# Kernel tuning notes

Hardware: AMD Instinct MI355X
Metric: run time of the kernel (lower is better)

## Reference

```python
import jax, jax.numpy as jnp
import numpy as np
from jax import lax

B, C, T = 64, 122, 500
COUT, D, H, FF, L = 64, 128, 8, 256, 2
NSUB, NCLS = 13, 4
EPS = 1e-5


def _gelu(x):
    return jax.nn.gelu(x, approximate=False)  # torch nn.GELU default (erf)


def _bn(x, g, b, m, v):
    # eval-mode BatchNorm1d over channel dim of [N, C, T]
    scale = (g / jnp.sqrt(v + EPS))[None, :, None]
    return (x - m[None, :, None]) * scale + b[None, :, None]


def _ln(x, g, b):
    mu = x.mean(-1, keepdims=True)
    var = ((x - mu) ** 2).mean(-1, keepdims=True)
    return (x - mu) / jnp.sqrt(var + EPS) * g + b


def _conv1d(x, w, b, pad):
    y = lax.conv_general_dilated(x, w, (1,), [(pad, pad)], dimension_numbers=('NCH', 'OIH', 'NCH'))
    return y + b[None, :, None]


def forward(x, subject_ids, conv1_w, conv1_b, bn1_g, bn1_b, bn1_m, bn1_v,
            conv2_w, conv2_b, bn2_g, bn2_b, bn2_m, bn2_v,
            proj_w, proj_b, elec_emb,
            qkv_w, qkv_b, out_w, out_b, ln1_g, ln1_b,
            ff1_w, ff1_b, ff2_w, ff2_b, ln2_g, ln2_b,
            heads_w, heads_b):
    bsz = x.shape[0]
    h = x.reshape(bsz * C, 1, T)                               # [B*C, 1, T]
    h = _gelu(_bn(_conv1d(h, conv1_w, conv1_b, 4), bn1_g, bn1_b, bn1_m, bn1_v))
    h = h.reshape(bsz * C, COUT, T // 2, 2).max(-1)            # MaxPool1d(2)
    h = _gelu(_bn(_conv1d(h, conv2_w, conv2_b, 2), bn2_g, bn2_b, bn2_m, bn2_v))
    h = h.mean(-1)                                             # AdaptiveAvgPool1d(1)
    tok = h @ proj_w.T + proj_b                                # [B*C, D]
    tok = tok.reshape(bsz, C, D) + elec_emb[:, :C, :]
    dh = D // H
    inv_sqrt_dh = 1.0 / float(np.sqrt(dh))
    for l in range(L):  # post-norm TransformerEncoderLayer, gelu activation
        qkv = jnp.einsum('bsd,ed->bse', tok, qkv_w[l]) + qkv_b[l]
        q, k, v = jnp.split(qkv, 3, axis=-1)
        q = q.reshape(bsz, C, H, dh)
        k = k.reshape(bsz, C, H, dh)
        v = v.reshape(bsz, C, H, dh)
        att = jax.nn.softmax(jnp.einsum('bqhd,bkhd->bhqk', q, k) * inv_sqrt_dh, axis=-1)
        ctx = jnp.einsum('bhqk,bkhd->bqhd', att, v).reshape(bsz, C, D)
        tok = _ln(tok + ctx @ out_w[l].T + out_b[l], ln1_g[l], ln1_b[l])
        ff = _gelu(tok @ ff1_w[l].T + ff1_b[l]) @ ff2_w[l].T + ff2_b[l]
        tok = _ln(tok + ff, ln2_g[l], ln2_b[l])
    pooled = tok.mean(axis=1)                                  # [B, D]
    # per-subject head routing == gather subject's weight/bias, batched matvec
    hw = heads_w[subject_ids]                                  # [B, NCLS, D]
    hb = heads_b[subject_ids]                                  # [B, NCLS]
    return jnp.einsum('bd,bcd->bc', pooled, hw) + hb


def setup_inputs() -> dict:
    key = jax.random.key(0)
    ks = jax.random.split(key, 16)
    def n(i, shape, s=0.02):
        return jax.random.normal(ks[i], shape, jnp.float32) * s
    return {
        'x': jax.random.normal(ks[0], (B, C, T), jnp.float32),
        'subject_ids': jax.random.randint(ks[1], (B,), 0, NSUB),
        'conv1_w': n(2, (COUT, 1, 9), 0.3), 'conv1_b': jnp.zeros((COUT,), jnp.float32),
        'bn1_g': jnp.ones((COUT,), jnp.float32), 'bn1_b': jnp.zeros((COUT,), jnp.float32),
        'bn1_m': jnp.zeros((COUT,), jnp.float32), 'bn1_v': jnp.ones((COUT,), jnp.float32),
        'conv2_w': n(3, (COUT, COUT, 5), 0.05), 'conv2_b': jnp.zeros((COUT,), jnp.float32),
        'bn2_g': jnp.ones((COUT,), jnp.float32), 'bn2_b': jnp.zeros((COUT,), jnp.float32),
        'bn2_m': jnp.zeros((COUT,), jnp.float32), 'bn2_v': jnp.ones((COUT,), jnp.float32),
        'proj_w': n(4, (D, COUT), 0.05), 'proj_b': jnp.zeros((D,), jnp.float32),
        'elec_emb': n(5, (1, C, D), 0.02),
        'qkv_w': n(6, (L, 3 * D, D), 0.05), 'qkv_b': jnp.zeros((L, 3 * D), jnp.float32),
        'out_w': n(7, (L, D, D), 0.05), 'out_b': jnp.zeros((L, D), jnp.float32),
        'ln1_g': jnp.ones((L, D), jnp.float32), 'ln1_b': jnp.zeros((L, D), jnp.float32),
        'ff1_w': n(8, (L, FF, D), 0.05), 'ff1_b': jnp.zeros((L, FF), jnp.float32),
        'ff2_w': n(9, (L, D, FF), 0.05), 'ff2_b': jnp.zeros((L, D), jnp.float32),
        'ln2_g': jnp.ones((L, D), jnp.float32), 'ln2_b': jnp.zeros((L, D), jnp.float32),
        'heads_w': n(10, (NSUB, NCLS, D), 0.05), 'heads_b': jnp.zeros((NSUB, NCLS), jnp.float32),
    }


def reference(x, subject_ids, conv1_w, conv1_b, bn1_g, bn1_b, bn1_m, bn1_v,
              conv2_w, conv2_b, bn2_g, bn2_b, bn2_m, bn2_v,
              proj_w, proj_b, elec_emb,
              qkv_w, qkv_b, out_w, out_b, ln1_g, ln1_b,
              ff1_w, ff1_b, ff2_w, ff2_b, ln2_g, ln2_b,
              heads_w, heads_b):
    return forward(x, subject_ids, conv1_w, conv1_b, bn1_g, bn1_b, bn1_m, bn1_v,
                   conv2_w, conv2_b, bn2_g, bn2_b, bn2_m, bn2_v,
                   proj_w, proj_b, elec_emb,
                   qkv_w, qkv_b, out_w, out_b, ln1_g, ln1_b,
                   ff1_w, ff1_b, ff2_w, ff2_b, ln2_g, ln2_b,
                   heads_w, heads_b)
```

## Files before the change

### kernel.cpp

```cpp
#include <hip/hip_runtime.h>
#include <hip/hip_fp16.h>
#include <hip/hip_bf16.h>
#include <math.h>

#define BB 64
#define CC 122
#define TT 500
#define NCOUT 64
#define DD 128
#define HHEADS 8
#define FFDIM 256
#define NLAYER 2
#define EPS 1e-5f
#define SEQ (BB*CC)

#define WS_W2T     0u
#define WS_PWT     10240u
#define WS_S1      20480u
#define WS_SH1     20544u
#define WS_S2      20608u
#define WS_SH2     20672u
#define WS_WBF     20736u
#define WS_TOK     151808u
#define WS_QKVB    1151232u
#define WS_VTB     2150656u
#define WS_GTAB    2674944u
#define WS_W1S     2675968u
#define WS_QKVB2   2676992u
#define WS_VTB2    3676416u

#define WB_QKV  0u
#define WB_OUT  98304u
#define WB_FF1  131072u
#define WB_FF2  196608u

typedef __attribute__((ext_vector_type(8))) short bf16x8;
typedef __attribute__((ext_vector_type(4))) float f32x4;

__device__ __forceinline__ unsigned short f2bf(float f) {
    unsigned int u = __float_as_uint(f);
    unsigned int r = u + 0x7FFFu + ((u >> 16) & 1u);
    return (unsigned short)(r >> 16);
}

__device__ __forceinline__ unsigned pk_bf16(float a, float b) {
    float r;
    asm("v_cvt_pk_bf16_f32 %0, %1, %2" : "=v"(r) : "v"(a), "v"(b));
    return __float_as_uint(r);
}
__device__ __forceinline__ unsigned short f2bf_hw(float f) {
    return (unsigned short)pk_bf16(f, f);
}

__device__ __forceinline__ float gelu_fast(float x) {
    float z = fabsf(x) * 0.70710678118654752f;
    float t = __builtin_amdgcn_rcpf(fmaf(0.3275911f, z, 1.0f));
    float p = fmaf(fmaf(fmaf(fmaf(1.061405429f, t, -1.453152027f), t,
                             1.421413741f), t, -0.284496736f), t, 0.254829592f);
    float e = __expf(-z * z);
    float erf_abs = fmaf(-p * t, e, 1.0f);
    float erf_x = copysignf(erf_abs, x);
    return 0.5f * x * (1.0f + erf_x);
}

__device__ __forceinline__ float gelu_idx(float p, const unsigned* __restrict__ gt) {
    p = fminf(fmaxf(p, 0.0f), 511.999f);
    int i = (int)p;
    float fr = p - (float)i;
    unsigned u = gt[i];
    __half2 h2 = *(__half2*)&u;
    float v0 = __half2float(h2.x);
    float d  = __half2float(h2.y);
    return fmaf(fr, d, v0);
}

__device__ __forceinline__ int swz3(int r) {
    return (r & 7) ^ (((r >> 4) & 1) << 1) ^ (((r >> 5) & 1) << 2);
}

__global__ void prep_kernel(const float* __restrict__ conv1_w, const float* __restrict__ conv1_b,
                            const float* __restrict__ bn1_g, const float* __restrict__ bn1_b,
                            const float* __restrict__ bn1_m, const float* __restrict__ bn1_v,
                            const float* __restrict__ conv2_w, const float* __restrict__ conv2_b,
                            const float* __restrict__ bn2_g, const float* __restrict__ bn2_b,
                            const float* __restrict__ bn2_m, const float* __restrict__ bn2_v,
                            const float* __restrict__ qkv_w, const float* __restrict__ out_w,
                            const float* __restrict__ ff1_w, const float* __restrict__ ff2_w,
                            const float* __restrict__ proj_w,
                            float* __restrict__ ws) {
    int idx = blockIdx.x * blockDim.x + threadIdx.x;
    if (idx < 20480) {
        int ci = idx & 63; int co = (idx >> 6) & 63; int kk = idx >> 12;
        unsigned short* wt = (unsigned short*)(ws + WS_W2T);
        wt[idx] = f2bf(conv2_w[(co*64 + ci)*5 + kk]);
    } else if (idx < 20544) {
        int i = idx - 20480;
        float s = bn1_g[i] * rsqrtf(bn1_v[i] + EPS);
        ws[WS_S1 + i] = s;
        ws[WS_SH1 + i] = (conv1_b[i] - bn1_m[i]) * s + bn1_b[i];
    } else if (idx < 20608) {
        int i = idx - 20544;
        float s = bn2_g[i] * rsqrtf(bn2_v[i] + EPS);
        ws[WS_S2 + i] = s;
        ws[WS_SH2 + i] = (conv2_b[i] - bn2_m[i]) * s + bn2_b[i];
    } else if (idx < 282752) {
        int r = idx - 20608;
        unsigned short* wbf = (unsigned short*)(ws + WS_WBF);
        float v;
        if (r < 98304)       v = qkv_w[r];
        else if (r < 131072) v = out_w[r - 98304];
        else if (r < 196608) v = ff1_w[r - 131072];
        else                 v = ff2_w[r - 196608];
        wbf[r] = f2bf(v);
    } else if (idx < 283264) {
        int i = idx - 282752;
        float x0 = (i - 256) * 0.03125f;
        float x1 = x0 + 0.03125f;
        float g0 = 0.5f*x0*(1.0f + erff(x0*0.70710678118654752f));
        float g1 = 0.5f*x1*(1.0f + erff(x1*0.70710678118654752f));
        __half hv = __float2half_rn(g0);
        __half hd = __float2half_rn(g1 - g0);
        unsigned short uv = *(unsigned short*)&hv;
        unsigned short ud = *(unsigned short*)&hd;
        ((unsigned*)(ws + WS_GTAB))[i] = (unsigned)uv | ((unsigned)ud << 16);
    } else if (idx < 285312) {
        int i = idx - 283264;
        int co = i >> 5, k = i & 31;
        unsigned short* w1s = (unsigned short*)(ws + WS_W1S);
        float s = bn1_g[co] * rsqrtf(bn1_v[co] + EPS);
        w1s[i] = (k < 9) ? f2bf(conv1_w[co*9 + k] * s) : (unsigned short)0;
    } else if (idx < 293504) {
        int i = idx - 285312;
        int o = i >> 7, d = i & 127;
        ws[WS_PWT + i] = proj_w[d*64 + o];
    }
}

__global__ __launch_bounds__(256, 4) void conv_kernel(const float* __restrict__ x,
            const float* __restrict__ proj_b,
            const float* __restrict__ elec,
            const float* __restrict__ wsr, float* __restrict__ tok) {
    __shared__ __align__(16) unsigned short h1s[264*64];
    __shared__ __align__(16) unsigned short xbf[544];
    __shared__ __align__(16) unsigned gtab[512];
    __shared__ float part[256];
    __shared__ float mean_l[64];
    int n = blockIdx.x;
    int c = n % CC;
    int tid = threadIdx.x;
    const float* xg = x + (size_t)n * TT;

    for (int i = tid; i < 544; i += 256) {
        unsigned short v = 0;
        if (i >= 4 && i < 504) v = f2bf_hw(xg[i-4]);
        xbf[i] = v;
    }
    if (tid < 128) {
        ((uint4*)gtab)[tid] = ((const uint4*)(wsr + WS_GTAB))[tid];
    }
    for (int idx = tid; idx < 14*64; idx += 256) {
        int rr = idx >> 6;
        int r = (rr < 2) ? rr : (rr - 2 + 252);
        h1s[r*64 + (idx & 63)] = 0;
    }
    __syncthreads();

    int lane = tid & 63;
    int w = tid >> 6;
    int ln15 = lane & 15, lg = lane >> 4;

    {
        const unsigned short* w1s = (const unsigned short*)(wsr + WS_W1S);
        bf16x8 b1f[4];
        float shp[4];
#pragma unroll
        for (int nt = 0; nt < 4; nt++) {
            int co = nt*16 + ln15;
            b1f[nt] = *(const bf16x8*)&w1s[co*32 + lg*8];
            shp[nt] = fmaf(wsr[WS_SH1 + co], 32.0f, 256.0f);
        }
        int P = w*128 + ln15*8 + lg*8;
        uint4 Va = *(const uint4*)&xbf[P];
        uint4 Vb = *(const uint4*)&xbf[P + 8];
        unsigned vwin[8] = {Va.x, Va.y, Va.z, Va.w, Vb.x, Vb.y, Vb.z, Vb.w};
#pragma unroll
        for (int a = 0; a < 4; a++) {
            union { unsigned u[4]; bf16x8 b; } Ue, Uo;
#pragma unroll
            for (int d = 0; d < 4; d++) {
                Ue.u[d] = vwin[a + d];
                Uo.u[d] = (vwin[a + d] >> 16) | (vwin[a + d + 1] << 16);
            }
            f32x4 ce[4], cod[4];
#pragma unroll
            for (int nt = 0; nt < 4; nt++) {
                ce[nt]  = __builtin_amdgcn_mfma_f32_16x16x32_bf16(Ue.b, b1f[nt],
                              (f32x4){0.f,0.f,0.f,0.f}, 0, 0, 0);
                cod[nt] = __builtin_amdgcn_mfma_f32_16x16x32_bf16(Uo.b, b1f[nt],
                              (f32x4){0.f,0.f,0.f,0.f}, 0, 0, 0);
            }
#pragma unroll
            for (int nt = 0; nt < 4; nt++) {
                int co = nt*16 + ln15;
#pragma unroll
                for (int i = 0; i < 4; i++) {
                    int tp = w*64 + lg*16 + i*4 + a;
                    if (tp < 250) {
                        float ge = gelu_idx(fmaf(ce[nt][i],  32.0f, shp[nt]), gtab);
                        float go = gelu_idx(fmaf(cod[nt][i], 32.0f, shp[nt]), gtab);
                        int r = tp + 2;
                        int cp = (co >> 3) ^ swz3(r);
                        h1s[r*64 + cp*8 + (co & 7)] = f2bf_hw(fmaxf(ge, go));
                    }
                }
            }
        }
    }
    __syncthreads();

    const unsigned short* wt = (const unsigned short*)(wsr + WS_W2T);
    f32x4 acc[4][4];
#pragma unroll
    for (int mi = 0; mi < 4; mi++)
#pragma unroll
        for (int nt = 0; nt < 4; nt++) acc[mi][nt] = (f32x4){0.f, 0.f, 0.f, 0.f};

    const unsigned short* wbase = wt + ln15*64 + lg*8;
#pragma unroll
    for (int kk = 0; kk < 5; kk++) {
#pragma unroll
        for (int s = 0; s < 2; s++) {
            bf16x8 bfv[4];
#pragma unroll
            for (int nt = 0; nt < 4; nt++)
                bfv[nt] = *(const bf16x8*)(wbase + kk*4096 + nt*1024 + s*32);
#pragma unroll
            for (int mi = 0; mi < 4; mi++) {
                int r = (w*4 + mi)*16 + ln15 + kk;
                int cp = (s*4 + lg) ^ swz3(r);
                bf16x8 af = *(const bf16x8*)&h1s[r*64 + cp*8];
#pragma unroll
                for (int nt = 0; nt < 4; nt++)
                    acc[mi][nt] = __builtin_amdgcn_mfma_f32_16x16x32_bf16(af, bfv[nt], acc[mi][nt], 0, 0, 0);
            }
        }
    }

#pragma unroll
    for (int nt = 0; nt < 4; nt++) {
        int co2 = nt*16 + ln15;
        float sc = wsr[WS_S2 + co2] * 32.0f;
        float sh = fmaf(wsr[WS_SH2 + co2], 32.0f, 256.0f);
        float p = 0.f;
#pragma unroll
        for (int mi = 0; mi < 4; mi++) {
            int tbase = (w*4 + mi)*16 + lg*4;
#pragma unroll
            for (int i = 0; i < 4; i++) {
                if (tbase + i < 250)
                    p += gelu_idx(fmaf(acc[mi][nt][i], sc, sh), gtab);
            }
        }
        p += __shfl_down(p, 32, 64);
        p += __shfl_down(p, 16, 64);
        if (lane < 16) part[w*64 + co2] = p;
    }
    __syncthreads();
    if (tid < 64) {
        mean_l[tid] = (part[tid] + part[64+tid] + part[128+tid] + part[192+tid]) * (1.0f/250.0f);
    }
    __syncthreads();

    if (tid < DD) {
        int d = tid;
        const float* pwt = wsr + WS_PWT;
        float a = proj_b[d] + elec[c*DD + d];
#pragma unroll 8
        for (int o = 0; o < 64; o++) a = fmaf(mean_l[o], pwt[o*128 + d], a);
        tok[(size_t)n * DD + d] = a;
    }
}

__global__ __launch_bounds__(256) void qkv_gemm(const float* __restrict__ Aptr,
        const unsigned short* __restrict__ Bbf,
        const float* __restrict__ bias,
        unsigned short* __restrict__ qkvb,
        unsigned short* __restrict__ vtb) {
    const int tid = threadIdx.x;
    const int m0 = blockIdx.x * 32;
    const int y  = blockIdx.y;
    const int n0 = y * 128;
    __shared__ __align__(16) unsigned short As[32*128];

    const float* A = Aptr + (size_t)m0 * 128;
    for (int i = tid; i < 1024; i += 256) {
        int m = i >> 5; int kq = (i & 31)*4;
        float4 v = *(const float4*)(A + m*128 + kq);
        int cp = (kq >> 3) ^ (m & 15);
        unsigned p0 = pk_bf16(v.x, v.y);
        unsigned p1 = pk_bf16(v.z, v.w);
        *(uint2*)&As[m*128 + cp*8 + (kq & 7)] = make_uint2(p0, p1);
    }
    __syncthreads();

    const int lane = tid & 63, w = tid >> 6;
    const int ln15 = lane & 15, lg = lane >> 4;
    f32x4 acc[2][2];
#pragma unroll
    for (int mi = 0; mi < 2; mi++)
#pragma unroll
        for (int ni = 0; ni < 2; ni++) acc[mi][ni] = (f32x4){0.f, 0.f, 0.f, 0.f};

    const unsigned short* Bb = Bbf + (size_t)n0 * 128;
#pragma unroll
    for (int kt = 0; kt < 4; kt++) {
        bf16x8 af[2], bfv[2];
#pragma unroll
        for (int mi = 0; mi < 2; mi++) {
            int m = mi*16 + ln15;
            int cp = (kt*4 + lg) ^ (m & 15);
            af[mi] = *(const bf16x8*)&As[m*128 + cp*8];
        }
#pragma unroll
        for (int ni = 0; ni < 2; ni++) {
            int nn = (w*2 + ni)*16 + ln15;
            bfv[ni] = *(const bf16x8*)&Bb[(size_t)nn*128 + kt*32 + lg*8];
        }
#pragma unroll
        for (int mi = 0; mi < 2; mi++)
#pragma unroll
            for (int ni = 0; ni < 2; ni++)
                acc[mi][ni] = __builtin_amdgcn_mfma_f32_16x16x32_bf16(af[mi], bfv[ni], acc[mi][ni], 0, 0, 0);
    }

#pragma unroll
    for (int mi = 0; mi < 2; mi++)
#pragma unroll
        for (int ni = 0; ni < 2; ni++) {
            int nloc = (w*2 + ni)*16 + ln15;
            float bb = bias[n0 + nloc];
#pragma unroll
            for (int i = 0; i < 4; i++) {
                int ml = mi*16 + lg*4 + i;
                int nrow = m0 + ml;
                unsigned short us = f2bf_hw(acc[mi][ni][i] + bb);
                if (y < 2) {
                    qkvb[(size_t)nrow*256 + n0 + nloc] = us;
                } else {
                    int bq = nrow / 122;
                    int j  = nrow - bq*122;
                    vtb[((size_t)(bq*128 + nloc))*128 + j] = us;
                }
            }
        }
}

__global__ __launch_bounds__(512) void attn_tail(
        const unsigned short* __restrict__ qkvb,
        const unsigned short* __restrict__ vtb,
        const unsigned short* __restrict__ outW, const float* __restrict__ outb,
        float* __restrict__ tok,
        const float* __restrict__ ln1g, const float* __restrict__ ln1b,
        const unsigned short* __restrict__ B1, const float* __restrict__ b1,
        const unsigned short* __restrict__ B2, const float* __restrict__ b2,
        const float* __restrict__ ln2g, const float* __restrict__ ln2b,
        const unsigned short* __restrict__ Bq, const float* __restrict__ bq,
        unsigned short* __restrict__ qkvb_o, unsigned short* __restrict__ vtb_o,
        int do_qkv) {
    __shared__ float Cs[16*129];
    __shared__ __align__(16) unsigned short Pregion[8*16*128];
    __shared__ __align__(16) unsigned short ctxs[16*128];

    const int tid = threadIdx.x;
    const int blk = blockIdx.x;
    const int b = blk >> 3, mq = blk & 7;
    const int m0l = mq * 16;
    const int lane = tid & 63, w = tid >> 6;
    const int ln15 = lane & 15, lg = lane >> 4;

    const unsigned short* qb = qkvb + (size_t)b * 122 * 256;
    unsigned short* Pw = Pregion + w * 2048;

    {
        const int h = w;
        int mrow = m0l + ln15;
        int gr = (mrow < 122) ? mrow : 121;
        bf16x8 af = {0,0,0,0,0,0,0,0};
        if (lg < 2) af = *(const bf16x8*)(qb + gr*256 + h*16 + lg*8);
        f32x4 S[8];
#pragma unroll
        for (int nt = 0; nt < 8; nt++) {
            int j = nt*16 + ln15;
            int gj = (j < 122) ? j : 121;
            bf16x8 bv = {0,0,0,0,0,0,0,0};
            if (lg < 2) bv = *(const bf16x8*)(qb + gj*256 + 128 + h*16 + lg*8);
            S[nt] = __builtin_amdgcn_mfma_f32_16x16x32_bf16(af, bv,
                        (f32x4){0.f,0.f,0.f,0.f}, 0, 0, 0);
        }
        float sm[4];
#pragma unroll
        for (int i = 0; i < 4; i++) {
            float m_ = -1e30f;
#pragma unroll
            for (int nt = 0; nt < 8; nt++) {
                float v = S[nt][i] * 0.25f;
                if (nt == 7 && ln15 >= 10) v = -1e30f;
                S[nt][i] = v;
                m_ = fmaxf(m_, v);
            }
            m_ = fmaxf(m_, __shfl_xor(m_, 1, 64));
            m_ = fmaxf(m_, __shfl_xor(m_, 2, 64));
            m_ = fmaxf(m_, __shfl_xor(m_, 4, 64));
            m_ = fmaxf(m_, __shfl_xor(m_, 8, 64));
            float s_ = 0.f;
#pragma unroll
            for (int nt = 0; nt < 8; nt++) {
                float e = __expf(S[nt][i] - m_);
                S[nt][i] = e;
                s_ += e;
            }
            s_ += __shfl_xor(s_, 1, 64);
            s_ += __shfl_xor(s_, 2, 64);
            s_ += __shfl_xor(s_, 4, 64);
            s_ += __shfl_xor(s_, 8, 64);
            sm[i] = s_;
        }
#pragma unroll
        for (int nt = 0; nt < 8; nt++)
#pragma unroll
            for (int i = 0; i < 4; i++) {
                int rp = lg*4 + i;
                int j = nt*16 + ln15;
                int cp = (j >> 3) ^ rp;
                Pw[rp*128 + cp*8 + (j & 7)] = f2bf_hw(S[nt][i]);
            }
        f32x4 cacc = (f32x4){0.f,0.f,0.f,0.f};
#pragma unroll
        for (int kt = 0; kt < 4; kt++) {
            bf16x8 bv = *(const bf16x8*)(vtb + ((size_t)(b*128 + h*16 + ln15))*128 + kt*32 + lg*8);
            int m = ln15;
            int cp = (kt*4 + lg) ^ m;
            bf16x8 ap = *(const bf16x8*)&Pw[m*128 + cp*8];
            cacc = __builtin_amdgcn_mfma_f32_16x16x32_bf16(ap, bv, cacc, 0, 0, 0);
        }
#pragma unroll
        for (int i = 0; i < 4; i++) {
            float inv = __builtin_amdgcn_rcpf(sm[i]);
            int rp = lg*4 + i;
            int ccol = h*16 + ln15;
            int cp = (ccol >> 3) ^ (rp & 15);
            ctxs[rp*128 + cp*8 + (ccol & 7)] = f2bf_hw(cacc[i] * inv);
        }
    }
    __syncthreads();

    {
        f32x4 acc = (f32x4){0.f,0.f,0.f,0.f};
        int nn = w*16 + ln15;
#pragma unroll
        for (int kt = 0; kt < 4; kt++) {
            bf16x8 bv = *(const bf16x8*)&outW[(size_t)nn*128 + kt*32 + lg*8];
            int m = ln15;
            int cp = (kt*4 + lg) ^ (m & 15);
            bf16x8 afm = *(const bf16x8*)&ctxs[m*128 + cp*8];
            acc = __builtin_amdgcn_mfma_f32_16x16x32_bf16(afm, bv, acc, 0, 0, 0);
        }
        float bb = outb[nn];
#pragma unroll
        for (int i = 0; i < 4; i++) {
            int ml = lg*4 + i;
            int mrow = m0l + ml;
            int grow = b*122 + ((mrow < 122) ? mrow : 121);
            Cs[ml*129 + nn] = acc[i] + bb + tok[(size_t)grow*128 + nn];
        }
    }
    __syncthreads();

    unsigned short* ln1buf = Pregion;
    unsigned short* Hs = Pregion + 2048;
    {
        int r = tid >> 5, sub = tid & 31;
        float s1 = 0.f, s2 = 0.f;
#pragma unroll
        for (int j = 0; j < 4; j++) {
            float vv = Cs[r*129 + sub*4 + j];
            s1 += vv; s2 += vv*vv;
        }
        s1 += __shfl_xor(s1, 1, 64);  s2 += __shfl_xor(s2, 1, 64);
        s1 += __shfl_xor(s1, 2, 64);  s2 += __shfl_xor(s2, 2, 64);
        s1 += __shfl_xor(s1, 4, 64);  s2 += __shfl_xor(s2, 4, 64);
        s1 += __shfl_xor(s1, 8, 64);  s2 += __shfl_xor(s2, 8, 64);
        s1 += __shfl_xor(s1, 16, 64); s2 += __shfl_xor(s2, 16, 64);
        float mu = s1 * (1.0f/128.0f);
        float var = s2 * (1.0f/128.0f) - mu*mu;
        float rstd = rsqrtf(var + EPS);
#pragma unroll
        for (int j = 0; j < 4; j++) {
            int nloc = sub*4 + j;
            float vv = (Cs[r*129 + nloc] - mu) * rstd * ln1g[nloc] + ln1b[nloc];
            Cs[r*129 + nloc] = vv;
            int cp = (nloc >> 3) ^ (r & 15);
            ln1buf[r*128 + cp*8 + (nloc & 7)] = f2bf_hw(vv);
        }
    }
    __syncthreads();

    {
        f32x4 acc1[2];
#pragma unroll
        for (int ni = 0; ni < 2; ni++) acc1[ni] = (f32x4){0.f,0.f,0.f,0.f};
#pragma unroll
        for (int kt = 0; kt < 4; kt++) {
            int m = ln15;
            int cp = (kt*4 + lg) ^ (m & 15);
            bf16x8 afm = *(const bf16x8*)&ln1buf[m*128 + cp*8];
#pragma unroll
            for (int ni = 0; ni < 2; ni++) {
                int nn = (w*2 + ni)*16 + ln15;
                bf16x8 bv = *(const bf16x8*)&B1[(size_t)nn*128 + kt*32 + lg*8];
                acc1[ni] = __builtin_amdgcn_mfma_f32_16x16x32_bf16(afm, bv, acc1[ni], 0, 0, 0);
            }
        }
#pragma unroll
        for (int ni = 0; ni < 2; ni++) {
            int nn = (w*2 + ni)*16 + ln15;
            float bb = b1[nn];
#pragma unroll
            for (int i = 0; i < 4; i++) {
                int m = lg*4 + i;
                float v = gelu_fast(acc1[ni][i] + bb);
                int cp = (nn >> 3) ^ (m & 15);
                Hs[m*256 + cp*8 + (nn & 7)] = f2bf_hw(v);
            }
        }
    }
    __syncthreads();

    {
        f32x4 acc2 = (f32x4){0.f,0.f,0.f,0.f};
        int nn = w*16 + ln15;
#pragma unroll
        for (int kt = 0; kt < 8; kt++) {
            bf16x8 bv = *(const bf16x8*)&B2[(size_t)nn*256 + kt*32 + lg*8];
            int m = ln15;
            int cp = (kt*4 + lg) ^ (m & 15);
            bf16x8 afm = *(const bf16x8*)&Hs[m*256 + cp*8];
            acc2 = __builtin_amdgcn_mfma_f32_16x16x32_bf16(afm, bv, acc2, 0, 0, 0);
        }
        float bb = b2[nn];
#pragma unroll
        for (int i = 0; i < 4; i++) {
            int ml = lg*4 + i;
            Cs[ml*129 + nn] = acc2[i] + bb + Cs[ml*129 + nn];
        }
    }
    __syncthreads();

    {
        int r = tid >> 5, sub = tid & 31;
        float s1 = 0.f, s2 = 0.f;
#pragma unroll
        for (int j = 0; j < 4; j++) {
            float vv = Cs[r*129 + sub*4 + j];
            s1 += vv; s2 += vv*vv;
        }
        s1 += __shfl_xor(s1, 1, 64);  s2 += __shfl_xor(s2, 1, 64);
        s1 += __shfl_xor(s1, 2, 64);  s2 += __shfl_xor(s2, 2, 64);
        s1 += __shfl_xor(s1, 4, 64);  s2 += __shfl_xor(s2, 4, 64);
        s1 += __shfl_xor(s1, 8, 64);  s2 += __shfl_xor(s2, 8, 64);
        s1 += __shfl_xor(s1, 16, 64); s2 += __shfl_xor(s2, 16, 64);
        float mu = s1 * (1.0f/128.0f);
        float var = s2 * (1.0f/128.0f) - mu*mu;
        float rstd = rsqrtf(var + EPS);
        bool rowok = (m0l + r < 122);
#pragma unroll
        for (int j = 0; j < 4; j++) {
            int nloc = sub*4 + j;
            float vv = (Cs[r*129 + nloc] - mu) * rstd * ln2g[nloc] + ln2b[nloc];
            if (rowok)
                tok[((size_t)(b*122 + m0l + r))*128 + nloc] = vv;
            if (do_qkv) {
                int cp = (nloc >> 3) ^ (r & 15);
                Pregion[r*128 + cp*8 + (nloc & 7)] = f2bf_hw(vv);
            }
        }
    }

    if (do_qkv) {
        __syncthreads();
        const unsigned short* qbuf = Pregion;
        f32x4 accq[3];
#pragma unroll
        for (int ni = 0; ni < 3; ni++) accq[ni] = (f32x4){0.f,0.f,0.f,0.f};
#pragma unroll
        for (int kt = 0; kt < 4; kt++) {
            int m = ln15;
            int cp = (kt*4 + lg) ^ (m & 15);
            bf16x8 afm = *(const bf16x8*)&qbuf[m*128 + cp*8];
#pragma unroll
            for (int ni = 0; ni < 3; ni++) {
                int e = w*48 + ni*16 + ln15;
                bf16x8 bv = *(const bf16x8*)&Bq[(size_t)e*128 + kt*32 + lg*8];
                accq[ni] = __builtin_amdgcn_mfma_f32_16x16x32_bf16(afm, bv, accq[ni], 0, 0, 0);
            }
        }
#pragma unroll
        for (int ni = 0; ni < 3; ni++) {
            int e = w*48 + ni*16 + ln15;
            float bb = bq[e];
#pragma unroll
            for (int i = 0; i < 4; i++) {
                int ml = lg*4 + i;
                int mrow = m0l + ml;
                if (mrow < 122) {
                    unsigned short us = f2bf_hw(accq[ni][i] + bb);
                    int nrow = b*122 + mrow;
                    if (e < 256)
                        qkvb_o[(size_t)nrow*256 + e] = us;
                    else
                        vtb_o[((size_t)(b*128 + (e - 256)))*128 + mrow] = us;
                }
            }
        }
    }
}

__global__ __launch_bounds__(512) void final_kernel(const float* __restrict__ tok,
        const int* __restrict__ sid,
        const float* __restrict__ hw, const float* __restrict__ hb,
        float* __restrict__ outp) {
    __shared__ float pool[4][DD];
    __shared__ float pooled[DD];
    int b = blockIdx.x, tid = threadIdx.x;
    int q = tid >> 7, d = tid & 127;
    float s = 0.f;
    for (int c2 = q; c2 < CC; c2 += 4) s += tok[((size_t)b*CC + c2)*DD + d];
    pool[q][d] = s;
    __syncthreads();
    if (tid < DD)
        pooled[tid] = (pool[0][tid] + pool[1][tid] + pool[2][tid] + pool[3][tid])
                      * (1.0f/(float)CC);
    __syncthreads();
    if (tid < 4) {
        int sb = sid[b];
        const float* w = hw + ((size_t)sb*4 + tid)*DD;
        float a = hb[sb*4 + tid];
#pragma unroll 8
        for (int d2 = 0; d2 < DD; d2++) a = fmaf(pooled[d2], w[d2], a);
        outp[b*4 + tid] = a;
    }
}

extern "C" void kernel_launch(void* const* d_in, const int* in_sizes, int n_in,
                              void* d_out, int out_size, void* d_ws, size_t ws_size,
                              hipStream_t stream) {
    const float* x       = (const float*)d_in[0];
    const int*   sid     = (const int*)  d_in[1];
    const float* conv1_w = (const float*)d_in[2];
    const float* conv1_b = (const float*)d_in[3];
    const float* bn1_g   = (const float*)d_in[4];
    const float* bn1_b   = (const float*)d_in[5];
    const float* bn1_m   = (const float*)d_in[6];
    const float* bn1_v   = (const float*)d_in[7];
    const float* conv2_w = (const float*)d_in[8];
    const float* conv2_b = (const float*)d_in[9];
    const float* bn2_g   = (const float*)d_in[10];
    const float* bn2_b   = (const float*)d_in[11];
    const float* bn2_m   = (const float*)d_in[12];
    const float* bn2_v   = (const float*)d_in[13];
    const float* proj_w  = (const float*)d_in[14];
    const float* proj_b  = (const float*)d_in[15];
    const float* elec    = (const float*)d_in[16];
    const float* qkv_w   = (const float*)d_in[17];
    const float* qkv_b   = (const float*)d_in[18];
    const float* out_w   = (const float*)d_in[19];
    const float* out_b   = (const float*)d_in[20];
    const float* ln1_g   = (const float*)d_in[21];
    const float* ln1_b   = (const float*)d_in[22];
    const float* ff1_w   = (const float*)d_in[23];
    const float* ff1_b   = (const float*)d_in[24];
    const float* ff2_w   = (const float*)d_in[25];
    const float* ff2_b   = (const float*)d_in[26];
    const float* ln2_g   = (const float*)d_in[27];
    const float* ln2_b   = (const float*)d_in[28];
    const float* heads_w = (const float*)d_in[29];
    const float* heads_b = (const float*)d_in[30];
    float* ws = (float*)d_ws;
    const unsigned short* wbf = (const unsigned short*)(ws + WS_WBF);
    unsigned short* qkvb  = (unsigned short*)(ws + WS_QKVB);
    unsigned short* vtb   = (unsigned short*)(ws + WS_VTB);
    unsigned short* qkvb2 = (unsigned short*)(ws + WS_QKVB2);
    unsigned short* vtb2  = (unsigned short*)(ws + WS_VTB2);

    prep_kernel<<<(293504 + 255)/256, 256, 0, stream>>>(
        conv1_w, conv1_b, bn1_g, bn1_b, bn1_m, bn1_v,
        conv2_w, conv2_b, bn2_g, bn2_b, bn2_m, bn2_v,
        qkv_w, out_w, ff1_w, ff2_w, proj_w, ws);

    conv_kernel<<<SEQ, 256, 0, stream>>>(x, proj_b, elec, ws, ws + WS_TOK);

    qkv_gemm<<<dim3(244,3), 256, 0, stream>>>(
        ws + WS_TOK, wbf + WB_QKV, qkv_b, qkvb, vtb);

    attn_tail<<<BB*8, 512, 0, stream>>>(
        qkvb, vtb,
        wbf + WB_OUT, out_b,
        ws + WS_TOK, ln1_g, ln1_b,
        wbf + WB_FF1, ff1_b,
        wbf + WB_FF2, ff2_b,
        ln2_g, ln2_b,
        wbf + WB_QKV + 49152, qkv_b + 384, qkvb2, vtb2, 1);

    attn_tail<<<BB*8, 512, 0, stream>>>(
        qkvb2, vtb2,
        wbf + WB_OUT + 16384, out_b + 128,
        ws + WS_TOK, ln1_g + 128, ln1_b + 128,
        wbf + WB_FF1 + 32768, ff1_b + 256,
        wbf + WB_FF2 + 32768, ff2_b + 128,
        ln2_g + 128, ln2_b + 128,
        wbf + WB_QKV, qkv_b, qkvb2, vtb2, 0);

    final_kernel<<<BB, 512, 0, stream>>>(ws + WS_TOK, sid, heads_w, heads_b, (float*)d_out);
}
```

Baseline: 411.3 us.

## Fuse layer-0 QKV projection into conv kernel epilogue, drop separate GEMM

```diff
diff --git a/kernel.cpp b/kernel.cpp
--- a/kernel.cpp
+++ b/kernel.cpp
@@ -50,6 +50,10 @@
 }
 __device__ __forceinline__ unsigned short f2bf_hw(float f) {
     return (unsigned short)pk_bf16(f, f);
+}
+
+__device__ __forceinline__ float bf2f(unsigned short u) {
+    return __uint_as_float(((unsigned)u) << 16);
 }
 
 __device__ __forceinline__ float gelu_fast(float x) {
@@ -139,12 +143,18 @@
 __global__ __launch_bounds__(256, 4) void conv_kernel(const float* __restrict__ x,
             const float* __restrict__ proj_b,
             const float* __restrict__ elec,
-            const float* __restrict__ wsr, float* __restrict__ tok) {
+            const float* __restrict__ wsr,
+            const unsigned short* __restrict__ qkvw,
+            const float* __restrict__ qkvbias,
+            unsigned short* __restrict__ qkvb,
+            unsigned short* __restrict__ vtb,
+            float* __restrict__ tok) {
     __shared__ __align__(16) unsigned short h1s[264*64];
     __shared__ __align__(16) unsigned short xbf[544];
     __shared__ __align__(16) unsigned gtab[512];
     __shared__ float part[256];
     __shared__ float mean_l[64];
+    __shared__ __align__(16) float rowb[DD];
     int n = blockIdx.x;
     int c = n % CC;
     int tid = threadIdx.x;
@@ -278,81 +288,44 @@
 #pragma unroll 8
         for (int o = 0; o < 64; o++) a = fmaf(mean_l[o], pwt[o*128 + d], a);
         tok[(size_t)n * DD + d] = a;
-    }
-}
-
-__global__ __launch_bounds__(256) void qkv_gemm(const float* __restrict__ Aptr,
-        const unsigned short* __restrict__ Bbf,
-        const float* __restrict__ bias,
-        unsigned short* __restrict__ qkvb,
-        unsigned short* __restrict__ vtb) {
-    const int tid = threadIdx.x;
-    const int m0 = blockIdx.x * 32;
-    const int y  = blockIdx.y;
-    const int n0 = y * 128;
-    __shared__ __align__(16) unsigned short As[32*128];
-
-    const float* A = Aptr + (size_t)m0 * 128;
-    for (int i = tid; i < 1024; i += 256) {
-        int m = i >> 5; int kq = (i & 31)*4;
-        float4 v = *(const float4*)(A + m*128 + kq);
-        int cp = (kq >> 3) ^ (m & 15);
-        unsigned p0 = pk_bf16(v.x, v.y);
-        unsigned p1 = pk_bf16(v.z, v.w);
-        *(uint2*)&As[m*128 + cp*8 + (kq & 7)] = make_uint2(p0, p1);
-    }
-    __syncthreads();
-
-    const int lane = tid & 63, w = tid >> 6;
-    const int ln15 = lane & 15, lg = lane >> 4;
-    f32x4 acc[2][2];
-#pragma unroll
-    for (int mi = 0; mi < 2; mi++)
-#pragma unroll
-        for (int ni = 0; ni < 2; ni++) acc[mi][ni] = (f32x4){0.f, 0.f, 0.f, 0.f};
-
-    const unsigned short* Bb = Bbf + (size_t)n0 * 128;
-#pragma unroll
-    for (int kt = 0; kt < 4; kt++) {
-        bf16x8 af[2], bfv[2];
-#pragma unroll
-        for (int mi = 0; mi < 2; mi++) {
-            int m = mi*16 + ln15;
-            int cp = (kt*4 + lg) ^ (m & 15);
-            af[mi] = *(const bf16x8*)&As[m*128 + cp*8];
-        }
-#pragma unroll
-        for (int ni = 0; ni < 2; ni++) {
-            int nn = (w*2 + ni)*16 + ln15;
-            bfv[ni] = *(const bf16x8*)&Bb[(size_t)nn*128 + kt*32 + lg*8];
-        }
-#pragma unroll
-        for (int mi = 0; mi < 2; mi++)
-#pragma unroll
-            for (int ni = 0; ni < 2; ni++)
-                acc[mi][ni] = __builtin_amdgcn_mfma_f32_16x16x32_bf16(af[mi], bfv[ni], acc[mi][ni], 0, 0, 0);
-    }
-
-#pragma unroll
-    for (int mi = 0; mi < 2; mi++)
-#pragma unroll
-        for (int ni = 0; ni < 2; ni++) {
-            int nloc = (w*2 + ni)*16 + ln15;
-            float bb = bias[n0 + nloc];
-#pragma unroll
-            for (int i = 0; i < 4; i++) {
-                int ml = mi*16 + lg*4 + i;
-                int nrow = m0 + ml;
-                unsigned short us = f2bf_hw(acc[mi][ni][i] + bb);
-                if (y < 2) {
-                    qkvb[(size_t)nrow*256 + n0 + nloc] = us;
-                } else {
-                    int bq = nrow / 122;
-                    int j  = nrow - bq*122;
-                    vtb[((size_t)(bq*128 + nloc))*128 + j] = us;
-                }
-            }
-        }
+        rowb[d] = bf2f(f2bf_hw(a));
+    }
+    __syncthreads();
+
+    {
+        int bq = n / 122;
+        int j  = n - bq*122;
+        float a2 = qkvbias[tid];
+        float a3 = qkvbias[256 + (tid & 127)];
+        const unsigned short* w1r = qkvw + (size_t)tid * 128;
+        const unsigned short* w2r = qkvw + (size_t)(256 + (tid & 127)) * 128;
+#pragma unroll 2
+        for (int k = 0; k < 128; k += 8) {
+            float4 rA = *(const float4*)&rowb[k];
+            float4 rB = *(const float4*)&rowb[k + 4];
+            bf16x8 wa = *(const bf16x8*)&w1r[k];
+            bf16x8 wb = *(const bf16x8*)&w2r[k];
+            a2 = fmaf(rA.x, bf2f((unsigned short)wa[0]), a2);
+            a2 = fmaf(rA.y, bf2f((unsigned short)wa[1]), a2);
+            a2 = fmaf(rA.z, bf2f((unsigned short)wa[2]), a2);
+            a2 = fmaf(rA.w, bf2f((unsigned short)wa[3]), a2);
+            a2 = fmaf(rB.x, bf2f((unsigned short)wa[4]), a2);
+            a2 = fmaf(rB.y, bf2f((unsigned short)wa[5]), a2);
+            a2 = fmaf(rB.z, bf2f((unsigned short)wa[6]), a2);
+            a2 = fmaf(rB.w, bf2f((unsigned short)wa[7]), a2);
+            a3 = fmaf(rA.x, bf2f((unsigned short)wb[0]), a3);
+            a3 = fmaf(rA.y, bf2f((unsigned short)wb[1]), a3);
+            a3 = fmaf(rA.z, bf2f((unsigned short)wb[2]), a3);
+            a3 = fmaf(rA.w, bf2f((unsigned short)wb[3]), a3);
+            a3 = fmaf(rB.x, bf2f((unsigned short)wb[4]), a3);
+            a3 = fmaf(rB.y, bf2f((unsigned short)wb[5]), a3);
+            a3 = fmaf(rB.z, bf2f((unsigned short)wb[6]), a3);
+            a3 = fmaf(rB.w, bf2f((unsigned short)wb[7]), a3);
+        }
+        qkvb[(size_t)n*256 + tid] = f2bf_hw(a2);
+        if (tid < 128)
+            vtb[((size_t)(bq*128 + tid))*128 + j] = f2bf_hw(a3);
+    }
 }
 
 __global__ __launch_bounds__(512) void attn_tail(
@@ -697,10 +670,8 @@
         conv2_w, conv2_b, bn2_g, bn2_b, bn2_m, bn2_v,
         qkv_w, out_w, ff1_w, ff2_w, proj_w, ws);
 
-    conv_kernel<<<SEQ, 256, 0, stream>>>(x, proj_b, elec, ws, ws + WS_TOK);
-
-    qkv_gemm<<<dim3(244,3), 256, 0, stream>>>(
-        ws + WS_TOK, wbf + WB_QKV, qkv_b, qkvb, vtb);
+    conv_kernel<<<SEQ, 256, 0, stream>>>(x, proj_b, elec, ws,
+        wbf + WB_QKV, qkv_b, qkvb, vtb, ws + WS_TOK);
 
     attn_tail<<<BB*8, 512, 0, stream>>>(
         qkvb, vtb,
```

Result: slower. 500.0 us (+21.6%).

## Split conv stage into two time chunks to halve LDS and accumulator footprint

Applied to the files above, without the earlier changes.

```diff
diff --git a/kernel.cpp b/kernel.cpp
--- a/kernel.cpp
+++ b/kernel.cpp
@@ -74,8 +74,12 @@
     return fmaf(fr, d, v0);
 }
 
-__device__ __forceinline__ int swz3(int r) {
-    return (r & 7) ^ (((r >> 4) & 1) << 1) ^ (((r >> 5) & 1) << 2);
+__device__ __forceinline__ unsigned ab16(unsigned hi, unsigned lo) {
+    return __builtin_amdgcn_alignbit(hi, lo, 16);
+}
+
+__device__ __forceinline__ int swzc(int r) {
+    return (r & 7) ^ (((r >> 3) & 1) << 1) ^ (((r >> 4) & 1) << 2);
 }
 
 __global__ void prep_kernel(const float* __restrict__ conv1_w, const float* __restrict__ conv1_b,
@@ -136,18 +140,126 @@
     }
 }
 
+template<int TB, int OFF, int NBC, int CH1>
+__device__ __forceinline__ void conv_chunk(
+        const unsigned short* __restrict__ xbf,
+        unsigned short* __restrict__ h1c,
+        const unsigned* __restrict__ gtab,
+        const float* __restrict__ wsr,
+        const unsigned short* __restrict__ wbase,
+        float (&psum)[4],
+        int tid, int w, int ln15, int lg) {
+    {
+        const unsigned short* w1s = (const unsigned short*)(wsr + WS_W1S);
+        bf16x8 b1f[4];
+        float shp[4];
+#pragma unroll
+        for (int nt = 0; nt < 4; nt++) {
+            int co = nt*16 + ln15;
+            b1f[nt] = *(const bf16x8*)&w1s[co*32 + lg*8];
+            shp[nt] = fmaf(wsr[WS_SH1 + co], 32.0f, 256.0f);
+        }
+        int P = TB + w*64 + ln15*4 + lg*8;
+        uint2 q0 = *(const uint2*)&xbf[P];
+        uint2 q1 = *(const uint2*)&xbf[P + 4];
+        uint2 q2 = *(const uint2*)&xbf[P + 8];
+        unsigned d0 = q0.x, d1 = q0.y, d2 = q1.x, d3 = q1.y, d4 = q2.x, d5 = q2.y;
+        unsigned e0 = ab16(d1,d0), e1 = ab16(d2,d1), e2 = ab16(d3,d2),
+                 e3 = ab16(d4,d3), e4 = ab16(d5,d4);
+        if (CH1 && tid < 128) h1c[126*64 + tid] = 0;
+#pragma unroll
+        for (int a = 0; a < 2; a++) {
+            union { unsigned u[4]; bf16x8 b; } Ue, Uo;
+            if (a == 0) {
+                Ue.u[0]=d0; Ue.u[1]=d1; Ue.u[2]=d2; Ue.u[3]=d3;
+                Uo.u[0]=e0; Uo.u[1]=e1; Uo.u[2]=e2; Uo.u[3]=e3;
+            } else {
+                Ue.u[0]=d1; Ue.u[1]=d2; Ue.u[2]=d3; Ue.u[3]=d4;
+                Uo.u[0]=e1; Uo.u[1]=e2; Uo.u[2]=e3; Uo.u[3]=e4;
+            }
+            f32x4 ce[4], cd[4];
+#pragma unroll
+            for (int nt = 0; nt < 4; nt++) {
+                ce[nt] = __builtin_amdgcn_mfma_f32_16x16x32_bf16(Ue.b, b1f[nt],
+                             (f32x4){0.f,0.f,0.f,0.f}, 0, 0, 0);
+                cd[nt] = __builtin_amdgcn_mfma_f32_16x16x32_bf16(Uo.b, b1f[nt],
+                             (f32x4){0.f,0.f,0.f,0.f}, 0, 0, 0);
+            }
+#pragma unroll
+            for (int nt = 0; nt < 4; nt++) {
+                int co = nt*16 + ln15;
+#pragma unroll
+                for (int i = 0; i < 4; i++) {
+                    int lr = w*32 + (lg*4 + i)*2 + a + OFF;
+                    if (CH1 == 0 || lr <= 125) {
+                        float ge = gelu_idx(fmaf(ce[nt][i], 32.0f, shp[nt]), gtab);
+                        float go = gelu_idx(fmaf(cd[nt][i], 32.0f, shp[nt]), gtab);
+                        int cp = (co >> 3) ^ swzc(lr);
+                        h1c[lr*64 + cp*8 + (co & 7)] = f2bf_hw(fmaxf(ge, go));
+                    }
+                }
+            }
+        }
+    }
+    __syncthreads();
+
+    f32x4 acc[2][4];
+#pragma unroll
+    for (int mi = 0; mi < 2; mi++)
+#pragma unroll
+        for (int nt = 0; nt < 4; nt++) acc[mi][nt] = (f32x4){0.f, 0.f, 0.f, 0.f};
+#pragma unroll
+    for (int kk = 0; kk < 5; kk++) {
+#pragma unroll
+        for (int s = 0; s < 2; s++) {
+            bf16x8 bfv[4];
+#pragma unroll
+            for (int nt = 0; nt < 4; nt++)
+                bfv[nt] = *(const bf16x8*)(wbase + kk*4096 + nt*1024 + s*32);
+#pragma unroll
+            for (int mi = 0; mi < 2; mi++) {
+                int lr = (w*2 + mi)*16 + ln15 + kk;
+                int cp = (s*4 + lg) ^ swzc(lr);
+                bf16x8 af = *(const bf16x8*)&h1c[lr*64 + cp*8];
+#pragma unroll
+                for (int nt = 0; nt < 4; nt++)
+                    acc[mi][nt] = __builtin_amdgcn_mfma_f32_16x16x32_bf16(af, bfv[nt], acc[mi][nt], 0, 0, 0);
+            }
+        }
+    }
+
+#pragma unroll
+    for (int nt = 0; nt < 4; nt++) {
+        int co = nt*16 + ln15;
+        float sc2 = wsr[WS_S2 + co] * 32.0f;
+        float sh2 = fmaf(wsr[WS_SH2 + co], 32.0f, 256.0f);
+        float p = 0.f;
+#pragma unroll
+        for (int mi = 0; mi < 2; mi++) {
+            int obase = (w*2 + mi)*16 + lg*4;
+#pragma unroll
+            for (int i = 0; i < 4; i++) {
+                if (obase + i < NBC)
+                    p += gelu_idx(fmaf(acc[mi][nt][i], sc2, sh2), gtab);
+            }
+        }
+        psum[nt] += p;
+    }
+    __syncthreads();
+}
+
 __global__ __launch_bounds__(256, 4) void conv_kernel(const float* __restrict__ x,
             const float* __restrict__ proj_b,
             const float* __restrict__ elec,
             const float* __restrict__ wsr, float* __restrict__ tok) {
-    __shared__ __align__(16) unsigned short h1s[264*64];
+    __shared__ __align__(16) unsigned short h1c[132*64];
     __shared__ __align__(16) unsigned short xbf[544];
     __shared__ __align__(16) unsigned gtab[512];
     __shared__ float part[256];
     __shared__ float mean_l[64];
-    int n = blockIdx.x;
-    int c = n % CC;
-    int tid = threadIdx.x;
+    const int n = blockIdx.x;
+    const int c = n % CC;
+    const int tid = threadIdx.x;
     const float* xg = x + (size_t)n * TT;
 
     for (int i = tid; i < 544; i += 256) {
@@ -158,112 +270,25 @@
     if (tid < 128) {
         ((uint4*)gtab)[tid] = ((const uint4*)(wsr + WS_GTAB))[tid];
     }
-    for (int idx = tid; idx < 14*64; idx += 256) {
-        int rr = idx >> 6;
-        int r = (rr < 2) ? rr : (rr - 2 + 252);
-        h1s[r*64 + (idx & 63)] = 0;
-    }
-    __syncthreads();
-
-    int lane = tid & 63;
-    int w = tid >> 6;
-    int ln15 = lane & 15, lg = lane >> 4;
-
-    {
-        const unsigned short* w1s = (const unsigned short*)(wsr + WS_W1S);
-        bf16x8 b1f[4];
-        float shp[4];
-#pragma unroll
-        for (int nt = 0; nt < 4; nt++) {
-            int co = nt*16 + ln15;
-            b1f[nt] = *(const bf16x8*)&w1s[co*32 + lg*8];
-            shp[nt] = fmaf(wsr[WS_SH1 + co], 32.0f, 256.0f);
-        }
-        int P = w*128 + ln15*8 + lg*8;
-        uint4 Va = *(const uint4*)&xbf[P];
-        uint4 Vb = *(const uint4*)&xbf[P + 8];
-        unsigned vwin[8] = {Va.x, Va.y, Va.z, Va.w, Vb.x, Vb.y, Vb.z, Vb.w};
-#pragma unroll
-        for (int a = 0; a < 4; a++) {
-            union { unsigned u[4]; bf16x8 b; } Ue, Uo;
-#pragma unroll
-            for (int d = 0; d < 4; d++) {
-                Ue.u[d] = vwin[a + d];
-                Uo.u[d] = (vwin[a + d] >> 16) | (vwin[a + d + 1] << 16);
-            }
-            f32x4 ce[4], cod[4];
-#pragma unroll
-            for (int nt = 0; nt < 4; nt++) {
-                ce[nt]  = __builtin_amdgcn_mfma_f32_16x16x32_bf16(Ue.b, b1f[nt],
-                              (f32x4){0.f,0.f,0.f,0.f}, 0, 0, 0);
-                cod[nt] = __builtin_amdgcn_mfma_f32_16x16x32_bf16(Uo.b, b1f[nt],
-                              (f32x4){0.f,0.f,0.f,0.f}, 0, 0, 0);
-            }
-#pragma unroll
-            for (int nt = 0; nt < 4; nt++) {
-                int co = nt*16 + ln15;
-#pragma unroll
-                for (int i = 0; i < 4; i++) {
-                    int tp = w*64 + lg*16 + i*4 + a;
-                    if (tp < 250) {
-                        float ge = gelu_idx(fmaf(ce[nt][i],  32.0f, shp[nt]), gtab);
-                        float go = gelu_idx(fmaf(cod[nt][i], 32.0f, shp[nt]), gtab);
-                        int r = tp + 2;
-                        int cp = (co >> 3) ^ swz3(r);
-                        h1s[r*64 + cp*8 + (co & 7)] = f2bf_hw(fmaxf(ge, go));
-                    }
-                }
-            }
-        }
-    }
-    __syncthreads();
-
-    const unsigned short* wt = (const unsigned short*)(wsr + WS_W2T);
-    f32x4 acc[4][4];
-#pragma unroll
-    for (int mi = 0; mi < 4; mi++)
-#pragma unroll
-        for (int nt = 0; nt < 4; nt++) acc[mi][nt] = (f32x4){0.f, 0.f, 0.f, 0.f};
-
-    const unsigned short* wbase = wt + ln15*64 + lg*8;
-#pragma unroll
-    for (int kk = 0; kk < 5; kk++) {
-#pragma unroll
-        for (int s = 0; s < 2; s++) {
-            bf16x8 bfv[4];
-#pragma unroll
-            for (int nt = 0; nt < 4; nt++)
-                bfv[nt] = *(const bf16x8*)(wbase + kk*4096 + nt*1024 + s*32);
-#pragma unroll
-            for (int mi = 0; mi < 4; mi++) {
-                int r = (w*4 + mi)*16 + ln15 + kk;
-                int cp = (s*4 + lg) ^ swz3(r);
-                bf16x8 af = *(const bf16x8*)&h1s[r*64 + cp*8];
-#pragma unroll
-                for (int nt = 0; nt < 4; nt++)
-                    acc[mi][nt] = __builtin_amdgcn_mfma_f32_16x16x32_bf16(af, bfv[nt], acc[mi][nt], 0, 0, 0);
-            }
-        }
-    }
+    if (tid < 128) { h1c[tid] = 0; h1c[130*64 + tid] = 0; }
+    __syncthreads();
+
+    const int lane = tid & 63;
+    const int w = tid >> 6;
+    const int ln15 = lane & 15, lg = lane >> 4;
+
+    const unsigned short* wbase = (const unsigned short*)(wsr + WS_W2T) + ln15*64 + lg*8;
+    float psum[4] = {0.f, 0.f, 0.f, 0.f};
+
+    conv_chunk<0,   2, 126, 0>(xbf, h1c, gtab, wsr, wbase, psum, tid, w, ln15, lg);
+    conv_chunk<248, 0, 124, 1>(xbf, h1c, gtab, wsr, wbase, psum, tid, w, ln15, lg);
 
 #pragma unroll
     for (int nt = 0; nt < 4; nt++) {
-        int co2 = nt*16 + ln15;
-        float sc = wsr[WS_S2 + co2] * 32.0f;
-        float sh = fmaf(wsr[WS_SH2 + co2], 32.0f, 256.0f);
-        float p = 0.f;
-#pragma unroll
-        for (int mi = 0; mi < 4; mi++) {
-            int tbase = (w*4 + mi)*16 + lg*4;
-#pragma unroll
-            for (int i = 0; i < 4; i++) {
-                if (tbase + i < 250)
-                    p += gelu_idx(fmaf(acc[mi][nt][i], sc, sh), gtab);
-            }
-        }
+        float p = psum[nt];
         p += __shfl_down(p, 32, 64);
         p += __shfl_down(p, 16, 64);
-        if (lane < 16) part[w*64 + co2] = p;
+        if (lane < 16) part[w*64 + nt*16 + ln15] = p;
     }
     __syncthreads();
     if (tid < 64) {
```

Result: slower. 620.5 us (+50.9%).
